# Kernel tuning notes

Measured on AMD Instinct MI355X. Metric: run time of the kernel, lower is better.

The kernel has to match this reference:

```python
import jax, jax.numpy as jnp
import numpy as np

BIG = 1e6  # sentinel larger than any image coordinate


def _edt_sq(mask):
    """Exact squared Euclidean distance transform of a 2D bool mask.

    Returns, for every pixel, the squared distance to the nearest True pixel.
    Separable algorithm: exact 1D EDT along axis 0 (two cummax scans), then a
    brute-force-but-vectorized lower-envelope min along axis 1.
    """
    H, W = mask.shape

    def nearest_below(m):
        # distance (along axis 0) to nearest True at index <= i, per column
        idx = jnp.arange(H, dtype=jnp.float32)[:, None]
        pos = jnp.where(m, idx, -BIG)
        return idx - jax.lax.cummax(pos, axis=0)

    d_down = nearest_below(mask)
    d_up = nearest_below(mask[::-1])[::-1]
    d1 = jnp.minimum(jnp.minimum(d_down, d_up), BIG)  # [H, W] axis-0 distance
    f = d1 * d1  # squared

    j = jnp.arange(W, dtype=jnp.float32)
    offs = (j[:, None] - j[None, :]) ** 2  # [W_out, W_k]
    # D[i,j] = min_k ( (j-k)^2 + f[i,k] )   -> [H, W, W] intermediate
    return jnp.min(f[:, None, :] + offs[None, :, :], axis=-1)


def _hausdorff_one(a, b):
    """Symmetric Hausdorff distance between bool masks a, b ([H, W]).
    NaN if either mask is empty (matches scipy/monai behaviour handled by loss)."""
    dt_b = jnp.sqrt(_edt_sq(b))  # distance of every pixel to set b
    dt_a = jnp.sqrt(_edt_sq(a))
    h_ab = jnp.max(jnp.where(a, dt_b, 0.0))  # max_{x in a} d(x, b)
    h_ba = jnp.max(jnp.where(b, dt_a, 0.0))
    hd = jnp.maximum(h_ab, h_ba)
    empty = jnp.logical_or(~jnp.any(a), ~jnp.any(b))
    return jnp.where(empty, jnp.nan, hd)


def setup_inputs() -> dict:
    key = jax.random.key(0)
    k1, k2 = jax.random.split(key)
    inputs = jax.random.uniform(k1, (8, 512, 512), dtype=jnp.float32)
    targets = jax.random.uniform(k2, (8, 512, 512), dtype=jnp.float32)
    return {"inputs": inputs, "targets": targets}


def reference(inputs, targets):
    a = inputs > 0.5
    b = targets > 0.5
    # sequential over batch to bound the [H, W, W] EDT intermediate
    hds = jax.lax.map(lambda ab: _hausdorff_one(ab[0], ab[1]), (a, b))
    # NaN (empty mask) -> 1, else 1 - 1/(1 + hd)
    to_mean = jnp.where(jnp.isnan(hds), 1.0, 1.0 - 1.0 / (1.0 + hds))
    return jnp.mean(to_mean)
```

## Files before the change

### kernel.cpp

```cpp
#include <hip/hip_runtime.h>
#include <hip/hip_bf16.h>

static constexpr int H = 512;
static constexpr int W = 512;
static constexpr int NIMG = 8;


static constexpr int NEGS = -20000;
static constexpr int POSS =  20000;

__global__ __launch_bounds__(512)
void k_col_edt(const float* __restrict__ A, const float* __restrict__ B,
               unsigned int* __restrict__ bm, unsigned int* __restrict__ cc,
               float* __restrict__ maxsq, int* __restrict__ anyflag,
               int* __restrict__ done, int* __restrict__ gdone) {
    const int tid  = threadIdx.x;
    const int quad = tid & 7;
    const int seg  = tid >> 3;
    const int sub  = seg & 3;
    const int win  = seg >> 2;
    const int cg   = blockIdx.x;
    const int m16  = blockIdx.y;

    if (cg == 0 && m16 == 0) {
        if (tid < 16)       { maxsq[tid] = 0.0f; anyflag[tid] = 0; }
        else if (tid < 32)  { done[(tid - 16) * 32] = 0; }
        else if (tid == 32) { *gdone = 0; }
    }

    const int colbase = cg * 32 + quad * 4;
    const float* src = (m16 < NIMG) ? (A + (size_t)m16 * H * W)
                                    : (B + (size_t)(m16 - NIMG) * H * W);
    const int row0 = seg * 8;
    const int w0   = win * 32;

    unsigned int m0 = 0, m1 = 0, m2 = 0, m3 = 0;
    #pragma unroll
    for (int r = 0; r < 8; ++r) {
        float4 v = *reinterpret_cast<const float4*>(src + (size_t)(row0 + r) * W + colbase);
        m0 |= (v.x > 0.5f ? 1u : 0u) << r;
        m1 |= (v.y > 0.5f ? 1u : 0u) << r;
        m2 |= (v.z > 0.5f ? 1u : 0u) << r;
        m3 |= (v.w > 0.5f ? 1u : 0u) << r;
    }

    const int sh = 8 * sub;
    m0 <<= sh; m1 <<= sh; m2 <<= sh; m3 <<= sh;
    m0 |= __shfl_xor(m0, 8, 64);  m0 |= __shfl_xor(m0, 16, 64);
    m1 |= __shfl_xor(m1, 8, 64);  m1 |= __shfl_xor(m1, 16, 64);
    m2 |= __shfl_xor(m2, 8, 64);  m2 |= __shfl_xor(m2, 16, 64);
    m3 |= __shfl_xor(m3, 8, 64);  m3 |= __shfl_xor(m3, 16, 64);

    __shared__ int s_hi[16][32];
    __shared__ int s_lo[16][32];
    if (sub == 0) {
        int4 hi, lo;
        hi.x = m0 ? (w0 + 31 - __clz((int)m0)) : NEGS;
        hi.y = m1 ? (w0 + 31 - __clz((int)m1)) : NEGS;
        hi.z = m2 ? (w0 + 31 - __clz((int)m2)) : NEGS;
        hi.w = m3 ? (w0 + 31 - __clz((int)m3)) : NEGS;
        lo.x = m0 ? (w0 + __ffs((int)m0) - 1) : POSS;
        lo.y = m1 ? (w0 + __ffs((int)m1) - 1) : POSS;
        lo.z = m2 ? (w0 + __ffs((int)m2) - 1) : POSS;
        lo.w = m3 ? (w0 + __ffs((int)m3) - 1) : POSS;
        *reinterpret_cast<int4*>(&s_hi[win][quad * 4]) = hi;
        *reinterpret_cast<int4*>(&s_lo[win][quad * 4]) = lo;
        uint4 o = make_uint4(m0, m1, m2, m3);
        *reinterpret_cast<uint4*>(&bm[((size_t)m16 * 16 + win) * W + colbase]) = o;
    }
    __syncthreads();

    if (sub == 0) {
        int4 cdn = {NEGS, NEGS, NEGS, NEGS};
        for (int t = 0; t < win; ++t) {
            int4 h = *reinterpret_cast<int4*>(&s_hi[t][quad * 4]);
            cdn.x = max(cdn.x, h.x); cdn.y = max(cdn.y, h.y);
            cdn.z = max(cdn.z, h.z); cdn.w = max(cdn.w, h.w);
        }
        int4 cup = {POSS, POSS, POSS, POSS};
        for (int t = win + 1; t < 16; ++t) {
            int4 l = *reinterpret_cast<int4*>(&s_lo[t][quad * 4]);
            cup.x = min(cup.x, l.x); cup.y = min(cup.y, l.y);
            cup.z = min(cup.z, l.z); cup.w = min(cup.w, l.w);
        }
        uint4 pk;
        pk.x = ((unsigned)cdn.x & 0xFFFFu) | ((unsigned)cup.x << 16);
        pk.y = ((unsigned)cdn.y & 0xFFFFu) | ((unsigned)cup.y << 16);
        pk.z = ((unsigned)cdn.z & 0xFFFFu) | ((unsigned)cup.z << 16);
        pk.w = ((unsigned)cdn.w & 0xFFFFu) | ((unsigned)cup.w << 16);
        *reinterpret_cast<uint4*>(&cc[((size_t)m16 * 16 + win) * W + colbase]) = pk;
    }
}

__global__ __launch_bounds__(512)
void k_row_env(const unsigned int* __restrict__ bm, const unsigned int* __restrict__ cc,
               float* __restrict__ maxsq, int* __restrict__ anyflag,
               int* __restrict__ done, int* __restrict__ gdone,
               float* __restrict__ out) {
    const int task = blockIdx.y;
    const int rg   = blockIdx.x;
    const int img  = task & 7;
    const int dir  = task >> 3;
    const int wave = threadIdx.x >> 6;
    const int lane = threadIdx.x & 63;
    const int fsel = (dir == 0) ? (NIMG + img) : img;
    const int msel = (dir == 0) ? img : (NIMG + img);
    const int p0 = lane * 8;
    const int w0 = rg * 32;

    __shared__ float sf[8][512];
    __shared__ float s_wmax[8];
    __shared__ int   s_wany[8];

    const unsigned int* brow = bm + ((size_t)msel * 16 + rg) * W + p0;
    uint4 b0 = *reinterpret_cast<const uint4*>(brow);
    uint4 b1 = *reinterpret_cast<const uint4*>(brow + 4);
    const unsigned int* erow = bm + ((size_t)fsel * 16 + rg) * W + p0;
    uint4 e0 = *reinterpret_cast<const uint4*>(erow);
    uint4 e1 = *reinterpret_cast<const uint4*>(erow + 4);
    const unsigned int* crow = cc + ((size_t)fsel * 16 + rg) * W + p0;
    uint4 c0 = *reinterpret_cast<const uint4*>(crow);
    uint4 c1 = *reinterpret_cast<const uint4*>(crow + 4);

    unsigned int mw[8] = {e0.x, e0.y, e0.z, e0.w, e1.x, e1.y, e1.z, e1.w};
    unsigned int mb[8] = {b0.x, b0.y, b0.z, b0.w, b1.x, b1.y, b1.z, b1.w};
    int cd[8], cu[8];
    {
        unsigned int cwv[8] = {c0.x, c0.y, c0.z, c0.w, c1.x, c1.y, c1.z, c1.w};
        #pragma unroll
        for (int e = 0; e < 8; ++e) {
            cd[e] = (int)(short)(cwv[e] & 0xFFFFu);
            cu[e] = (int)(short)(cwv[e] >> 16);
        }
    }

    float vmax = 0.0f;
    int   vany = 0;

    #pragma unroll 1
    for (int it = 0; it < 4; ++it) {
        const int bit = it * 8 + wave;
        const int row = w0 + bit;

        float w[24];
        #pragma unroll
        for (int e = 0; e < 8; ++e) {
            unsigned int below = mw[e] & (0xFFFFFFFFu >> (31 - bit));
            int pos_dn = below ? (w0 + 31 - __clz((int)below)) : cd[e];
            unsigned int above = mw[e] & (0xFFFFFFFFu << bit);
            int pos_up = above ? (w0 + __ffs((int)above) - 1) : cu[e];
            int d = min(row - pos_dn, pos_up - row);
            w[8 + e] = (float)(d * d);
        }

        #pragma unroll
        for (int e = 0; e < 8; ++e) {
            w[e]      = __shfl_up(w[8 + e], 1, 64);
            w[16 + e] = __shfl_down(w[8 + e], 1, 64);
        }
        if (lane == 0) {
            #pragma unroll
            for (int e = 0; e < 8; ++e) w[e] = 1.0e12f;
        }
        if (lane == 63) {
            #pragma unroll
            for (int e = 0; e < 8; ++e) w[16 + e] = 1.0e12f;
        }

        bool mk[8];
        #pragma unroll
        for (int e = 0; e < 8; ++e) mk[e] = (mb[e] >> bit) & 1u;
        #pragma unroll
        for (int p = 0; p < 8; ++p) vany |= (int)mk[p];

        float best[8];
        #pragma unroll
        for (int p = 0; p < 8; ++p) best[p] = w[8 + p];
        #pragma unroll
        for (int r = 1; r <= 8; ++r) {
            const float rr = (float)(r * r);
            #pragma unroll
            for (int p = 0; p < 8; ++p)
                best[p] = fminf(best[p], fminf(rr + w[8 + p - r], rr + w[8 + p + r]));
        }

        float bmax = 0.0f;
        #pragma unroll
        for (int p = 0; p < 8; ++p) bmax = fmaxf(bmax, mk[p] ? best[p] : 0.0f);
        if (!__all(bmax <= 81.0f)) {
            float* srow = &sf[wave][0];
            *reinterpret_cast<float4*>(srow + p0)     = make_float4(w[8],  w[9],  w[10], w[11]);
            *reinterpret_cast<float4*>(srow + p0 + 4) = make_float4(w[12], w[13], w[14], w[15]);
            for (int r = 9; r < W; ++r) {
                const float rr = (float)(r * r);
                if (__all(rr >= bmax)) break;
                #pragma unroll
                for (int p = 0; p < 8; ++p) {
                    int kl = p0 + p - r, kr = p0 + p + r;
                    float cl = (kl >= 0) ? srow[kl] : 1.0e12f;
                    float cr = (kr < W)  ? srow[kr] : 1.0e12f;
                    best[p] = fminf(best[p], fminf(rr + cl, rr + cr));
                }
                bmax = 0.0f;
                #pragma unroll
                for (int p = 0; p < 8; ++p) bmax = fmaxf(bmax, mk[p] ? best[p] : 0.0f);
            }
        }

        #pragma unroll
        for (int p = 0; p < 8; ++p) vmax = fmaxf(vmax, mk[p] ? best[p] : 0.0f);
    }

    #pragma unroll
    for (int off = 32; off > 0; off >>= 1)
        vmax = fmaxf(vmax, __shfl_down(vmax, off, 64));
    int wany = __any(vany) ? 1 : 0;
    if (lane == 0) { s_wmax[wave] = vmax; s_wany[wave] = wany; }
    __syncthreads();
    if (threadIdx.x == 0) {
        float mx = s_wmax[0]; int af = s_wany[0];
        #pragma unroll
        for (int q = 1; q < 8; ++q) { mx = fmaxf(mx, s_wmax[q]); af |= s_wany[q]; }
        atomicMax((int*)&maxsq[task], __float_as_int(mx));
        if (af) atomicOr(&anyflag[msel], 1);
        asm volatile("s_waitcnt vmcnt(0)" ::: "memory");
        int p = atomicAdd(&done[task * 32], 1);
        if (p == (int)gridDim.x - 1) {
            int g = atomicAdd(gdone, 1);
            if (g == 15) {
                float s = 0.0f;
                for (int i2 = 0; i2 < NIMG; ++i2) {
                    int af1 = __hip_atomic_load(&anyflag[i2],        __ATOMIC_RELAXED, __HIP_MEMORY_SCOPE_AGENT);
                    int af2 = __hip_atomic_load(&anyflag[NIMG + i2], __ATOMIC_RELAXED, __HIP_MEMORY_SCOPE_AGENT);
                    float m1 = __hip_atomic_load(&maxsq[i2],         __ATOMIC_RELAXED, __HIP_MEMORY_SCOPE_AGENT);
                    float m2 = __hip_atomic_load(&maxsq[NIMG + i2],  __ATOMIC_RELAXED, __HIP_MEMORY_SCOPE_AGENT);
                    float loss;
                    if (!af1 || !af2) {
                        loss = 1.0f;
                    } else {
                        float hd = sqrtf(fmaxf(m1, m2));
                        loss = 1.0f - 1.0f / (1.0f + hd);
                    }
                    s += loss;
                }
                out[0] = s * (1.0f / (float)NIMG);
            }
        }
    }
}

extern "C" void kernel_launch(void* const* d_in, const int* in_sizes, int n_in,
                              void* d_out, int out_size, void* d_ws, size_t ws_size,
                              hipStream_t stream) {
    const float* A = (const float*)d_in[0];
    const float* B = (const float*)d_in[1];
    char* base = (char*)d_ws;
    float* maxsq      = (float*)(base + 0);
    int*   anyflag    = (int*)(base + 64);
    int*   done       = (int*)(base + 256);
    int*   gdone      = (int*)(base + 2304);
    unsigned int* bm  = (unsigned int*)(base + 4096);
    unsigned int* cc  = (unsigned int*)(base + 4096 + 512 * 1024);
    float* out        = (float*)d_out;

    hipLaunchKernelGGL(k_col_edt, dim3(W / 32, 16), dim3(512), 0, stream,
                       A, B, bm, cc, maxsq, anyflag, done, gdone);
    hipLaunchKernelGGL(k_row_env, dim3(16, 16), dim3(512), 0, stream,
                       bm, cc, maxsq, anyflag, done, gdone, out);
}
```

Before: 22.04 us.

## Fuse column EDT and row envelope into one cooperative kernel with per-image flags

Merges the two launches into a single cooperative kernel of 256 blocks. Each block first builds its column bitmask and nearest-row data, then raises a per-image completion counter. Before the row-envelope pass it spins until both masks it needs are complete. The final reduction is done by block 255 after polling all task counters, and the counters are now zeroed by a hipMemsetAsync before the launch. The aim is to remove the gap between kernel launches and let images proceed independently. In exchange it adds a memset node, cooperative-launch overhead and spin-wait latency.

```diff
diff --git a/kernel.cpp b/kernel.cpp
--- a/kernel.cpp
+++ b/kernel.cpp
@@ -10,109 +10,114 @@
 static constexpr int POSS =  20000;
 
 __global__ __launch_bounds__(512)
-void k_col_edt(const float* __restrict__ A, const float* __restrict__ B,
-               unsigned int* __restrict__ bm, unsigned int* __restrict__ cc,
-               float* __restrict__ maxsq, int* __restrict__ anyflag,
-               int* __restrict__ done, int* __restrict__ gdone) {
-    const int tid  = threadIdx.x;
-    const int quad = tid & 7;
-    const int seg  = tid >> 3;
-    const int sub  = seg & 3;
-    const int win  = seg >> 2;
-    const int cg   = blockIdx.x;
-    const int m16  = blockIdx.y;
-
-    if (cg == 0 && m16 == 0) {
-        if (tid < 16)       { maxsq[tid] = 0.0f; anyflag[tid] = 0; }
-        else if (tid < 32)  { done[(tid - 16) * 32] = 0; }
-        else if (tid == 32) { *gdone = 0; }
-    }
-
-    const int colbase = cg * 32 + quad * 4;
-    const float* src = (m16 < NIMG) ? (A + (size_t)m16 * H * W)
-                                    : (B + (size_t)(m16 - NIMG) * H * W);
-    const int row0 = seg * 8;
-    const int w0   = win * 32;
-
-    unsigned int m0 = 0, m1 = 0, m2 = 0, m3 = 0;
-    #pragma unroll
-    for (int r = 0; r < 8; ++r) {
-        float4 v = *reinterpret_cast<const float4*>(src + (size_t)(row0 + r) * W + colbase);
-        m0 |= (v.x > 0.5f ? 1u : 0u) << r;
-        m1 |= (v.y > 0.5f ? 1u : 0u) << r;
-        m2 |= (v.z > 0.5f ? 1u : 0u) << r;
-        m3 |= (v.w > 0.5f ? 1u : 0u) << r;
-    }
-
-    const int sh = 8 * sub;
-    m0 <<= sh; m1 <<= sh; m2 <<= sh; m3 <<= sh;
-    m0 |= __shfl_xor(m0, 8, 64);  m0 |= __shfl_xor(m0, 16, 64);
-    m1 |= __shfl_xor(m1, 8, 64);  m1 |= __shfl_xor(m1, 16, 64);
-    m2 |= __shfl_xor(m2, 8, 64);  m2 |= __shfl_xor(m2, 16, 64);
-    m3 |= __shfl_xor(m3, 8, 64);  m3 |= __shfl_xor(m3, 16, 64);
-
-    __shared__ int s_hi[16][32];
-    __shared__ int s_lo[16][32];
-    if (sub == 0) {
-        int4 hi, lo;
-        hi.x = m0 ? (w0 + 31 - __clz((int)m0)) : NEGS;
-        hi.y = m1 ? (w0 + 31 - __clz((int)m1)) : NEGS;
-        hi.z = m2 ? (w0 + 31 - __clz((int)m2)) : NEGS;
-        hi.w = m3 ? (w0 + 31 - __clz((int)m3)) : NEGS;
-        lo.x = m0 ? (w0 + __ffs((int)m0) - 1) : POSS;
-        lo.y = m1 ? (w0 + __ffs((int)m1) - 1) : POSS;
-        lo.z = m2 ? (w0 + __ffs((int)m2) - 1) : POSS;
-        lo.w = m3 ? (w0 + __ffs((int)m3) - 1) : POSS;
-        *reinterpret_cast<int4*>(&s_hi[win][quad * 4]) = hi;
-        *reinterpret_cast<int4*>(&s_lo[win][quad * 4]) = lo;
-        uint4 o = make_uint4(m0, m1, m2, m3);
-        *reinterpret_cast<uint4*>(&bm[((size_t)m16 * 16 + win) * W + colbase]) = o;
-    }
-    __syncthreads();
-
-    if (sub == 0) {
-        int4 cdn = {NEGS, NEGS, NEGS, NEGS};
-        for (int t = 0; t < win; ++t) {
-            int4 h = *reinterpret_cast<int4*>(&s_hi[t][quad * 4]);
-            cdn.x = max(cdn.x, h.x); cdn.y = max(cdn.y, h.y);
-            cdn.z = max(cdn.z, h.z); cdn.w = max(cdn.w, h.w);
-        }
-        int4 cup = {POSS, POSS, POSS, POSS};
-        for (int t = win + 1; t < 16; ++t) {
-            int4 l = *reinterpret_cast<int4*>(&s_lo[t][quad * 4]);
-            cup.x = min(cup.x, l.x); cup.y = min(cup.y, l.y);
-            cup.z = min(cup.z, l.z); cup.w = min(cup.w, l.w);
-        }
-        uint4 pk;
-        pk.x = ((unsigned)cdn.x & 0xFFFFu) | ((unsigned)cup.x << 16);
-        pk.y = ((unsigned)cdn.y & 0xFFFFu) | ((unsigned)cup.y << 16);
-        pk.z = ((unsigned)cdn.z & 0xFFFFu) | ((unsigned)cup.z << 16);
-        pk.w = ((unsigned)cdn.w & 0xFFFFu) | ((unsigned)cup.w << 16);
-        *reinterpret_cast<uint4*>(&cc[((size_t)m16 * 16 + win) * W + colbase]) = pk;
-    }
-}
-
-__global__ __launch_bounds__(512)
-void k_row_env(const unsigned int* __restrict__ bm, const unsigned int* __restrict__ cc,
-               float* __restrict__ maxsq, int* __restrict__ anyflag,
-               int* __restrict__ done, int* __restrict__ gdone,
-               float* __restrict__ out) {
-    const int task = blockIdx.y;
-    const int rg   = blockIdx.x;
-    const int img  = task & 7;
-    const int dir  = task >> 3;
-    const int wave = threadIdx.x >> 6;
-    const int lane = threadIdx.x & 63;
-    const int fsel = (dir == 0) ? (NIMG + img) : img;
-    const int msel = (dir == 0) ? img : (NIMG + img);
-    const int p0 = lane * 8;
-    const int w0 = rg * 32;
-
+void k_fused(const float* __restrict__ A, const float* __restrict__ B,
+             unsigned int* __restrict__ bm, unsigned int* __restrict__ cc,
+             float* __restrict__ maxsq, int* __restrict__ anyflag,
+             int* __restrict__ done, int* __restrict__ mask_done,
+             float* __restrict__ out) {
+    const int tid = threadIdx.x;
+    const int b   = blockIdx.x;
+
+    __shared__ int   s_hi[16][32];
+    __shared__ int   s_lo[16][32];
     __shared__ float sf[8][512];
     __shared__ float s_wmax[8];
     __shared__ int   s_wany[8];
 
-    const unsigned int* brow = bm + ((size_t)msel * 16 + rg) * W + p0;
+    {
+        const int quad = tid & 7;
+        const int seg  = tid >> 3;
+        const int sub  = seg & 3;
+        const int win  = seg >> 2;
+        const int cg   = b & 15;
+        const int m16  = b >> 4;
+
+        const int colbase = cg * 32 + quad * 4;
+        const float* src = (m16 < NIMG) ? (A + (size_t)m16 * H * W)
+                                        : (B + (size_t)(m16 - NIMG) * H * W);
+        const int row0 = seg * 8;
+        const int w0   = win * 32;
+
+        unsigned int m0 = 0, m1 = 0, m2 = 0, m3 = 0;
+        #pragma unroll
+        for (int r = 0; r < 8; ++r) {
+            float4 v = *reinterpret_cast<const float4*>(src + (size_t)(row0 + r) * W + colbase);
+            m0 |= (v.x > 0.5f ? 1u : 0u) << r;
+            m1 |= (v.y > 0.5f ? 1u : 0u) << r;
+            m2 |= (v.z > 0.5f ? 1u : 0u) << r;
+            m3 |= (v.w > 0.5f ? 1u : 0u) << r;
+        }
+
+        const int sh = 8 * sub;
+        m0 <<= sh; m1 <<= sh; m2 <<= sh; m3 <<= sh;
+        m0 |= __shfl_xor(m0, 8, 64);  m0 |= __shfl_xor(m0, 16, 64);
+        m1 |= __shfl_xor(m1, 8, 64);  m1 |= __shfl_xor(m1, 16, 64);
+        m2 |= __shfl_xor(m2, 8, 64);  m2 |= __shfl_xor(m2, 16, 64);
+        m3 |= __shfl_xor(m3, 8, 64);  m3 |= __shfl_xor(m3, 16, 64);
+
+        if (sub == 0) {
+            int4 hi, lo;
+            hi.x = m0 ? (w0 + 31 - __clz((int)m0)) : NEGS;
+            hi.y = m1 ? (w0 + 31 - __clz((int)m1)) : NEGS;
+            hi.z = m2 ? (w0 + 31 - __clz((int)m2)) : NEGS;
+            hi.w = m3 ? (w0 + 31 - __clz((int)m3)) : NEGS;
+            lo.x = m0 ? (w0 + __ffs((int)m0) - 1) : POSS;
+            lo.y = m1 ? (w0 + __ffs((int)m1) - 1) : POSS;
+            lo.z = m2 ? (w0 + __ffs((int)m2) - 1) : POSS;
+            lo.w = m3 ? (w0 + __ffs((int)m3) - 1) : POSS;
+            *reinterpret_cast<int4*>(&s_hi[win][quad * 4]) = hi;
+            *reinterpret_cast<int4*>(&s_lo[win][quad * 4]) = lo;
+            uint4 o = make_uint4(m0, m1, m2, m3);
+            *reinterpret_cast<uint4*>(&bm[((size_t)m16 * 16 + win) * W + colbase]) = o;
+        }
+        __syncthreads();
+
+        if (sub == 0) {
+            int4 cdn = {NEGS, NEGS, NEGS, NEGS};
+            for (int t = 0; t < win; ++t) {
+                int4 h = *reinterpret_cast<int4*>(&s_hi[t][quad * 4]);
+                cdn.x = max(cdn.x, h.x); cdn.y = max(cdn.y, h.y);
+                cdn.z = max(cdn.z, h.z); cdn.w = max(cdn.w, h.w);
+            }
+            int4 cup = {POSS, POSS, POSS, POSS};
+            for (int t = win + 1; t < 16; ++t) {
+                int4 l = *reinterpret_cast<int4*>(&s_lo[t][quad * 4]);
+                cup.x = min(cup.x, l.x); cup.y = min(cup.y, l.y);
+                cup.z = min(cup.z, l.z); cup.w = min(cup.w, l.w);
+            }
+            uint4 pk;
+            pk.x = ((unsigned)cdn.x & 0xFFFFu) | ((unsigned)cup.x << 16);
+            pk.y = ((unsigned)cdn.y & 0xFFFFu) | ((unsigned)cup.y << 16);
+            pk.z = ((unsigned)cdn.z & 0xFFFFu) | ((unsigned)cup.z << 16);
+            pk.w = ((unsigned)cdn.w & 0xFFFFu) | ((unsigned)cup.w << 16);
+            *reinterpret_cast<uint4*>(&cc[((size_t)m16 * 16 + win) * W + colbase]) = pk;
+        }
+    }
+
+    __syncthreads();
+    if (tid == 0)
+        __hip_atomic_fetch_add(&mask_done[(b >> 4) * 32], 1,
+                               __ATOMIC_RELEASE, __HIP_MEMORY_SCOPE_AGENT);
+
+    const int task = b >> 4;
+    const int rg   = b & 15;
+    const int fsel = task ^ 8;
+    const int wave = tid >> 6;
+    const int lane = tid & 63;
+    const int p0 = lane * 8;
+    const int w0 = rg * 32;
+
+    if (tid == 0) {
+        while (__hip_atomic_load(&mask_done[task * 32],
+                                 __ATOMIC_ACQUIRE, __HIP_MEMORY_SCOPE_AGENT) < 16)
+            __builtin_amdgcn_s_sleep(1);
+        while (__hip_atomic_load(&mask_done[fsel * 32],
+                                 __ATOMIC_ACQUIRE, __HIP_MEMORY_SCOPE_AGENT) < 16)
+            __builtin_amdgcn_s_sleep(1);
+    }
+    __syncthreads();
+
+    const unsigned int* brow = bm + ((size_t)task * 16 + rg) * W + p0;
     uint4 b0 = *reinterpret_cast<const uint4*>(brow);
     uint4 b1 = *reinterpret_cast<const uint4*>(brow + 4);
     const unsigned int* erow = bm + ((size_t)fsel * 16 + rg) * W + p0;
@@ -217,34 +222,35 @@
     int wany = __any(vany) ? 1 : 0;
     if (lane == 0) { s_wmax[wave] = vmax; s_wany[wave] = wany; }
     __syncthreads();
-    if (threadIdx.x == 0) {
+    if (tid == 0) {
         float mx = s_wmax[0]; int af = s_wany[0];
         #pragma unroll
         for (int q = 1; q < 8; ++q) { mx = fmaxf(mx, s_wmax[q]); af |= s_wany[q]; }
         atomicMax((int*)&maxsq[task], __float_as_int(mx));
-        if (af) atomicOr(&anyflag[msel], 1);
-        asm volatile("s_waitcnt vmcnt(0)" ::: "memory");
-        int p = atomicAdd(&done[task * 32], 1);
-        if (p == (int)gridDim.x - 1) {
-            int g = atomicAdd(gdone, 1);
-            if (g == 15) {
-                float s = 0.0f;
-                for (int i2 = 0; i2 < NIMG; ++i2) {
-                    int af1 = __hip_atomic_load(&anyflag[i2],        __ATOMIC_RELAXED, __HIP_MEMORY_SCOPE_AGENT);
-                    int af2 = __hip_atomic_load(&anyflag[NIMG + i2], __ATOMIC_RELAXED, __HIP_MEMORY_SCOPE_AGENT);
-                    float m1 = __hip_atomic_load(&maxsq[i2],         __ATOMIC_RELAXED, __HIP_MEMORY_SCOPE_AGENT);
-                    float m2 = __hip_atomic_load(&maxsq[NIMG + i2],  __ATOMIC_RELAXED, __HIP_MEMORY_SCOPE_AGENT);
-                    float loss;
-                    if (!af1 || !af2) {
-                        loss = 1.0f;
-                    } else {
-                        float hd = sqrtf(fmaxf(m1, m2));
-                        loss = 1.0f - 1.0f / (1.0f + hd);
-                    }
-                    s += loss;
+        if (af) atomicOr(&anyflag[task], 1);
+        __hip_atomic_fetch_add(&done[task * 32], 1,
+                               __ATOMIC_RELEASE, __HIP_MEMORY_SCOPE_AGENT);
+        if (b == 255) {
+            for (int t = 0; t < 16; ++t)
+                while (__hip_atomic_load(&done[t * 32],
+                                         __ATOMIC_ACQUIRE, __HIP_MEMORY_SCOPE_AGENT) < 16)
+                    __builtin_amdgcn_s_sleep(1);
+            float s = 0.0f;
+            for (int i2 = 0; i2 < NIMG; ++i2) {
+                int af1 = __hip_atomic_load(&anyflag[i2],        __ATOMIC_RELAXED, __HIP_MEMORY_SCOPE_AGENT);
+                int af2 = __hip_atomic_load(&anyflag[NIMG + i2], __ATOMIC_RELAXED, __HIP_MEMORY_SCOPE_AGENT);
+                float m1 = __hip_atomic_load(&maxsq[i2],         __ATOMIC_RELAXED, __HIP_MEMORY_SCOPE_AGENT);
+                float m2 = __hip_atomic_load(&maxsq[NIMG + i2],  __ATOMIC_RELAXED, __HIP_MEMORY_SCOPE_AGENT);
+                float loss;
+                if (!af1 || !af2) {
+                    loss = 1.0f;
+                } else {
+                    float hd = sqrtf(fmaxf(m1, m2));
+                    loss = 1.0f - 1.0f / (1.0f + hd);
                 }
-                out[0] = s * (1.0f / (float)NIMG);
-            }
+                s += loss;
+            }
+            out[0] = s * (1.0f / (float)NIMG);
         }
     }
 }
@@ -258,13 +264,15 @@
     float* maxsq      = (float*)(base + 0);
     int*   anyflag    = (int*)(base + 64);
     int*   done       = (int*)(base + 256);
-    int*   gdone      = (int*)(base + 2304);
-    unsigned int* bm  = (unsigned int*)(base + 4096);
-    unsigned int* cc  = (unsigned int*)(base + 4096 + 512 * 1024);
+    int*   mask_done  = (int*)(base + 2304);
+    unsigned int* bm  = (unsigned int*)(base + 8192);
+    unsigned int* cc  = (unsigned int*)(base + 8192 + 512 * 1024);
     float* out        = (float*)d_out;
 
-    hipLaunchKernelGGL(k_col_edt, dim3(W / 32, 16), dim3(512), 0, stream,
-                       A, B, bm, cc, maxsq, anyflag, done, gdone);
-    hipLaunchKernelGGL(k_row_env, dim3(16, 16), dim3(512), 0, stream,
-                       bm, cc, maxsq, anyflag, done, gdone, out);
+    hipMemsetAsync(base, 0, 8192, stream);
+
+    void* args[] = {(void*)&A, (void*)&B, (void*)&bm, (void*)&cc,
+                    (void*)&maxsq, (void*)&anyflag, (void*)&done,
+                    (void*)&mask_done, (void*)&out};
+    hipLaunchCooperativeKernel((void*)k_fused, dim3(256), dim3(512), args, 0, stream);
 }
```

Result: slower. 53.36 us (median of 2 runs) (+142.2%).
